# Optimization experiments

Measured on AMD Instinct MI355X. Metric: run time of the kernel, lower is better.

## Reference

```python
import jax, jax.numpy as jnp
import numpy as np

N = 8192
D = 128
AVG_DEG = 32


def setup_inputs() -> dict:
    key = jax.random.key(0)
    ks = jax.random.split(key, 10)
    Z = jax.random.normal(ks[0], (N, D), dtype=jnp.float32)
    # random symmetric binary adjacency with avg degree ~ AVG_DEG
    p = AVG_DEG / N
    adj = (jax.random.uniform(ks[1], (N, N)) < p).astype(jnp.float32)
    adj = jnp.maximum(adj, adj.T)
    # symmetric normalized adjacency: D^{-1/2} A D^{-1/2}
    deg = adj.sum(axis=1)
    d_inv_sqrt = jnp.where(deg > 0, 1.0 / jnp.sqrt(deg), 0.0)
    A_norm = d_inv_sqrt[:, None] * adj * d_inv_sqrt[None, :]
    sc = 1.0 / np.sqrt(D)
    W_D = jax.random.uniform(ks[2], (D, D), minval=-sc, maxval=sc, dtype=jnp.float32)
    W_C = jax.random.uniform(ks[3], (D, D), minval=-sc, maxval=sc, dtype=jnp.float32)
    w_V = jax.random.uniform(ks[4], (D,), minval=-sc, maxval=sc, dtype=jnp.float32)
    W1 = jax.random.uniform(ks[5], (D, D), minval=-sc, maxval=sc, dtype=jnp.float32)
    b1 = jax.random.uniform(ks[6], (D,), minval=-sc, maxval=sc, dtype=jnp.float32)
    W2 = jax.random.uniform(ks[7], (D, D), minval=-sc, maxval=sc, dtype=jnp.float32)
    b2 = jax.random.uniform(ks[8], (D,), minval=-sc, maxval=sc, dtype=jnp.float32)
    omega_logit = jnp.float32(0.0)  # sigmoid -> 0.5
    delta_logit = jnp.float32(0.0)
    return {"Z": Z, "A_norm": A_norm, "W_D": W_D, "W_C": W_C, "w_V": w_V,
            "W1": W1, "b1": b1, "W2": W2, "b2": b2,
            "omega_logit": omega_logit, "delta_logit": delta_logit}


def reference(Z, A_norm, W_D, W_C, w_V, W1, b1, W2, b2, omega_logit, delta_logit):
    omega = jax.nn.sigmoid(omega_logit)
    delta = jax.nn.sigmoid(delta_logit)
    # Diffusion: ReLU(A_norm @ Z @ W_D^T)
    dif = jax.nn.relu(A_norm @ (Z @ W_D.T))  # [N, D]
    # Convection (standard attention). Since W_V is D->1,
    # W_V(z_i - z_j) == s_i - s_j with s = Z @ w_V -> avoid [N,N,D] tensor.
    s = Z @ w_V                                   # [N]
    V_bar = jax.nn.sigmoid(s[:, None] - s[None, :])  # [N, N]
    A = jax.nn.softmax(V_bar, axis=1)                # row-stochastic [N, N]
    con = A @ (Z @ W_C.T)                            # [N, D]
    # Reaction: nonlinear MLP
    rea = jnp.tanh(Z @ W1.T + b1) @ W2.T + b2        # [N, D]
    return omega * dif + (1.0 - omega) * con + delta * rea
```

## Files before the change

### kernel.cpp

```cpp
#include <hip/hip_runtime.h>
#include <hip/hip_bf16.h>
#include <stdint.h>

#define NN 8192
#define DD 128
#define MAXDEG 128

typedef float f32x4 __attribute__((ext_vector_type(4)));
typedef __bf16 bf16x8 __attribute__((ext_vector_type(8)));
typedef __bf16 bf16x4 __attribute__((ext_vector_type(4)));

__device__ __forceinline__ f32x4 mfma16(bf16x8 a, bf16x8 b, f32x4 c) {
    return __builtin_amdgcn_mfma_f32_16x16x32_bf16(a, b, c, 0, 0, 0);
}

__device__ __forceinline__ bf16x8 pack8(f32x4 lo, f32x4 hi) {
    bf16x8 r;
    r[0] = (__bf16)lo[0]; r[1] = (__bf16)lo[1]; r[2] = (__bf16)lo[2]; r[3] = (__bf16)lo[3];
    r[4] = (__bf16)hi[0]; r[5] = (__bf16)hi[1]; r[6] = (__bf16)hi[2]; r[7] = (__bf16)hi[3];
    return r;
}

__device__ __forceinline__ float fast_sigmoid(float x) {
    return __builtin_amdgcn_rcpf(1.0f + __expf(-x));
}

__device__ __forceinline__ uint32_t f32_bf16bits_rne(float f) {
    union { float f; uint32_t u; } c; c.f = f;
    return (c.u + 0x7fffu + ((c.u >> 16) & 1u)) >> 16;
}

__device__ __forceinline__ float bf16bits_f32(uint32_t b) {
    union { uint32_t u; float f; } c; c.u = b << 16;
    return c.f;
}

__global__ __launch_bounds__(256) void k_prep_sE(
    const float* __restrict__ Z, const float* __restrict__ wV, float* __restrict__ E)
{
    const int wid  = threadIdx.x >> 6;
    const int lane = threadIdx.x & 63;
    const int row  = blockIdx.x * 4 + wid;
    float p = Z[row * DD + lane] * wV[lane] + Z[row * DD + 64 + lane] * wV[64 + lane];
    #pragma unroll
    for (int off = 32; off > 0; off >>= 1) p += __shfl_xor(p, off, 64);
    if (lane == 0) E[row] = __expf(p);
}

__global__ __launch_bounds__(256) void k_conv_w(
    const float* __restrict__ W_D, const float* __restrict__ W_C,
    const float* __restrict__ W1, const float* __restrict__ W2,
    __bf16* __restrict__ Wb)
{
    const int t = blockIdx.x * 256 + threadIdx.x;
    const int m = t >> 12, i = t & 4095;
    const float* src = (m == 0) ? W_D : (m == 1) ? W_C : (m == 2) ? W1 : W2;
    const f32x4 v = *(const f32x4*)(src + i * 4);
    bf16x4 b;
    b[0] = (__bf16)v[0]; b[1] = (__bf16)v[1]; b[2] = (__bf16)v[2]; b[3] = (__bf16)v[3];
    *(bf16x4*)(Wb + m * 16384 + i * 4) = b;
}

__global__ __launch_bounds__(256) void k_prep2(
    const float* __restrict__ Z, const __bf16* __restrict__ Wb,
    const float* __restrict__ b1, const float* __restrict__ b2,
    const float* __restrict__ delta_logit,
    __bf16* __restrict__ XR, __bf16* __restrict__ YB, __bf16* __restrict__ REA)
{
    __shared__ __bf16 Hs[32][136];
    const int tid = threadIdx.x;
    const int w = tid >> 6, l = tid & 63;
    const int lr = l & 15, lg = l >> 4;
    const int wr = w & 1, wn = w >> 1;
    const int r0 = blockIdx.x * 32;
    const int arow = r0 + 16 * wr + lr;
    const __bf16* WDb = Wb;
    const __bf16* WCb = Wb + 16384;
    const __bf16* W1b = Wb + 32768;
    const __bf16* W2b = Wb + 49152;

    const f32x4 zero4 = {0.f, 0.f, 0.f, 0.f};
    f32x4 aXD[4], aY[4], aH[4];
    #pragma unroll
    for (int i = 0; i < 4; ++i) { aXD[i] = zero4; aY[i] = zero4; aH[i] = zero4; }

    #pragma unroll
    for (int t = 0; t < 4; ++t) {
        const int k0 = 32 * t + 8 * lg;
        const bf16x8 af = pack8(*(const f32x4*)(Z + arow * DD + k0),
                                *(const f32x4*)(Z + arow * DD + k0 + 4));
        #pragma unroll
        for (int nf = 0; nf < 4; ++nf) {
            const int col = 64 * wn + 16 * nf + lr;
            aXD[nf] = mfma16(af, *(const bf16x8*)(WDb + col * DD + k0), aXD[nf]);
            aY[nf]  = mfma16(af, *(const bf16x8*)(WCb + col * DD + k0), aY[nf]);
            aH[nf]  = mfma16(af, *(const bf16x8*)(W1b + col * DD + k0), aH[nf]);
        }
    }

    const int orow = r0 + 16 * wr + 4 * lg;
    const int tile = orow >> 5;
    #pragma unroll
    for (int nf = 0; nf < 4; ++nf) {
        const int col = 64 * wn + 16 * nf + lr;
        bf16x4 yo;
        const float bb1 = b1[col];
        #pragma unroll
        for (int r = 0; r < 4; ++r) {
            XR[(orow + r) * DD + col] = (__bf16)aXD[nf][r];
            yo[r] = (__bf16)aY[nf][r];
            const float x = aH[nf][r] + bb1;
            const float e = __expf(2.0f * x);
            Hs[16 * wr + 4 * lg + r][col] = (__bf16)(1.0f - 2.0f * __builtin_amdgcn_rcpf(e + 1.0f));
        }
        *(bf16x4*)(YB + tile * 4096 + col * 32 + (orow & 31)) = yo;
    }
    __syncthreads();

    f32x4 aR[4];
    #pragma unroll
    for (int i = 0; i < 4; ++i) aR[i] = zero4;
    #pragma unroll
    for (int t = 0; t < 4; ++t) {
        const int k0 = 32 * t + 8 * lg;
        const bf16x8 hf = *(const bf16x8*)(&Hs[16 * wr + lr][k0]);
        #pragma unroll
        for (int nf = 0; nf < 4; ++nf) {
            const int col = 64 * wn + 16 * nf + lr;
            aR[nf] = mfma16(hf, *(const bf16x8*)(W2b + col * DD + k0), aR[nf]);
        }
    }
    const float delta = fast_sigmoid(delta_logit[0]);
    #pragma unroll
    for (int nf = 0; nf < 4; ++nf) {
        const int col = 64 * wn + 16 * nf + lr;
        const float bb2 = b2[col];
        #pragma unroll
        for (int r = 0; r < 4; ++r)
            REA[(orow + r) * DD + col] = (__bf16)(delta * (aR[nf][r] + bb2));
    }
}

__global__ __launch_bounds__(256) void k_scan(
    const float* __restrict__ A, uint32_t* __restrict__ cnt, uint32_t* __restrict__ ents)
{
    const int g = blockIdx.x * 256 + threadIdx.x;
    #pragma unroll 4
    for (int i = 0; i < 32; ++i) {
        const int idx4 = i * 524288 + g;
        const f32x4 v = *(const f32x4*)(A + (size_t)idx4 * 4);
        const float sm = (v[0] + v[1]) + (v[2] + v[3]);
        if (sm != 0.0f) {
            const int row = idx4 >> 11;
            const int colbase = (idx4 & 2047) * 4;
            #pragma unroll
            for (int k = 0; k < 4; ++k) {
                if (v[k] != 0.0f) {
                    const uint32_t slot = atomicAdd(&cnt[row], 1u);
                    if (slot < MAXDEG)
                        ents[row * MAXDEG + slot] =
                            ((uint32_t)(colbase + k) << 16) | f32_bf16bits_rne(v[k]);
                }
            }
        }
    }
}

__global__ __launch_bounds__(512) __attribute__((amdgpu_waves_per_eu(2, 2))) void k_con(
    const float* __restrict__ E, const __bf16* __restrict__ YB,
    const __bf16* __restrict__ XR, const __bf16* __restrict__ REA,
    const uint32_t* __restrict__ cnt, const uint32_t* __restrict__ ents,
    const float* __restrict__ omega_logit, float* __restrict__ out)
{
    __shared__ float red[4][64][76];
    float* conS = &red[0][0][0];
    const int tid = threadIdx.x;
    const int w = tid >> 6, l = tid & 63;
    const int lr = l & 15, lg = l >> 4;
    const int r0 = blockIdx.x * 32;
    const int kstart = w * 1024;

    const float* ep = E + kstart + 8 * lg;
    const __bf16* yp = YB + (kstart >> 5) * 4096 + lr * 32 + 8 * lg;
    const float u0 = E[r0 + lr];
    const float u1 = E[r0 + 16 + lr];

    const f32x4 zero4 = {0.f, 0.f, 0.f, 0.f};
    f32x4 aC0[8], aC1[8], aden0 = zero4, aden1 = zero4;
    #pragma unroll
    for (int i = 0; i < 8; ++i) { aC0[i] = zero4; aC1[i] = zero4; }
    bf16x8 ones;
    #pragma unroll
    for (int i = 0; i < 8; ++i) ones[i] = (__bf16)1.0f;

    f32x4 eAa, eBa, eAb, eBb;
    bf16x8 bya[8], byb[8];
    intptr_t adv = 32;

#define LOADT(S) do {                                                         \
        eA##S = *(const f32x4*)(ep); eB##S = *(const f32x4*)(ep + 4);         \
        _Pragma("unroll")                                                     \
        for (int c = 0; c < 8; ++c) by##S[c] = *(const bf16x8*)(yp + c * 512);\
        ep += adv; yp += adv * 128;                                           \
    } while (0)

#define COMPT(S) do {                                                         \
        bf16x8 gf0, gf1;                                                      \
        _Pragma("unroll")                                                     \
        for (int j = 0; j < 4; ++j) {                                         \
            const float ea = eA##S[j], eb = eB##S[j];                         \
            gf0[j]     = (__bf16)__expf(u0 * __builtin_amdgcn_rcpf(u0 + ea)); \
            gf0[4 + j] = (__bf16)__expf(u0 * __builtin_amdgcn_rcpf(u0 + eb)); \
            gf1[j]     = (__bf16)__expf(u1 * __builtin_amdgcn_rcpf(u1 + ea)); \
            gf1[4 + j] = (__bf16)__expf(u1 * __builtin_amdgcn_rcpf(u1 + eb)); \
        }                                                                     \
        _Pragma("unroll")                                                     \
        for (int c = 0; c < 8; ++c) {                                         \
            aC0[c] = mfma16(gf0, by##S[c], aC0[c]);                           \
            aC1[c] = mfma16(gf1, by##S[c], aC1[c]);                           \
        }                                                                     \
        aden0 = mfma16(gf0, ones, aden0);                                     \
        aden1 = mfma16(gf1, ones, aden1);                                     \
    } while (0)

    LOADT(a);
    for (int it = 0; it < 16; ++it) {
        if (it == 15) adv = 0;
        LOADT(b); COMPT(a);
        LOADT(a); COMPT(b);
    }
#undef LOADT
#undef COMPT

#define STORE_ACC(dst) do {                                                   \
        _Pragma("unroll")                                                     \
        for (int c = 0; c < 8; ++c) {                                         \
            *(f32x4*)((dst) + c * 4)      = aC0[c];                           \
            *(f32x4*)((dst) + 36 + c * 4) = aC1[c];                           \
        }                                                                     \
        *(f32x4*)((dst) + 32)      = aden0;                                   \
        *(f32x4*)((dst) + 36 + 32) = aden1;                                   \
    } while (0)
#define ADD_ACC(src) do {                                                     \
        _Pragma("unroll")                                                     \
        for (int c = 0; c < 8; ++c) {                                         \
            aC0[c] += *(const f32x4*)((src) + c * 4);                         \
            aC1[c] += *(const f32x4*)((src) + 36 + c * 4);                    \
        }                                                                     \
        aden0 += *(const f32x4*)((src) + 32);                                 \
        aden1 += *(const f32x4*)((src) + 36 + 32);                            \
    } while (0)

    if (w >= 4) STORE_ACC(&red[w - 4][l][0]);
    __syncthreads();
    if (w < 4) ADD_ACC(&red[w][l][0]);
    __syncthreads();
    if (w == 2 || w == 3) STORE_ACC(&red[w - 2][l][0]);
    __syncthreads();
    if (w < 2) ADD_ACC(&red[w][l][0]);
    __syncthreads();
    if (w == 1) STORE_ACC(&red[0][l][0]);
    __syncthreads();
    if (w == 0) {
        ADD_ACC(&red[0][l][0]);
        __builtin_amdgcn_s_barrier();
        #pragma unroll
        for (int rf = 0; rf < 2; ++rf) {
            #pragma unroll
            for (int c = 0; c < 8; ++c) {
                const f32x4 v = rf ? aC1[c] : aC0[c];
                #pragma unroll
                for (int r = 0; r < 4; ++r)
                    conS[(16 * rf + 4 * lg + r) * 132 + 16 * c + lr] = v[r];
            }
            if (lr == 0) {
                const f32x4 d = rf ? aden1 : aden0;
                #pragma unroll
                for (int r = 0; r < 4; ++r)
                    conS[32 * 132 + 16 * rf + 4 * lg + r] = d[r];
            }
        }
    } else {
        __builtin_amdgcn_s_barrier();
    }
    __syncthreads();

    const int row = tid >> 4;
    const int g16 = tid & 15;
    const int col0 = 8 * g16;
    const int rg = r0 + row;
    float acc[8];
    #pragma unroll
    for (int i = 0; i < 8; ++i) acc[i] = 0.0f;

    const uint32_t n = min(cnt[rg], (uint32_t)MAXDEG);
    const uint32_t* ep2 = ents + rg * MAXDEG;
    for (uint32_t e = 0; e < n; ++e) {
        const uint32_t p = ep2[e];
        const float val = bf16bits_f32(p & 0xffffu);
        const bf16x8 xv = *(const bf16x8*)(XR + (size_t)(p >> 16) * DD + col0);
        #pragma unroll
        for (int i = 0; i < 8; ++i) acc[i] += val * (float)xv[i];
    }

    const float omega = fast_sigmoid(omega_logit[0]);
    const float om1 = 1.0f - omega;
    const float dinv = __builtin_amdgcn_rcpf(conS[32 * 132 + row]);
    const bf16x8 rea8 = *(const bf16x8*)(REA + (size_t)rg * DD + col0);
    f32x4 o0, o1;
    #pragma unroll
    for (int i = 0; i < 8; ++i) {
        const float dv = fmaxf(acc[i], 0.0f);
        const float cv = conS[row * 132 + col0 + i] * dinv;
        const float v = (float)rea8[i] + omega * dv + om1 * cv;
        if (i < 4) o0[i] = v; else o1[i - 4] = v;
    }
    *(f32x4*)(out + (size_t)rg * DD + col0) = o0;
    *(f32x4*)(out + (size_t)rg * DD + col0 + 4) = o1;
}

extern "C" void kernel_launch(void* const* d_in, const int* in_sizes, int n_in,
                              void* d_out, int out_size, void* d_ws, size_t ws_size,
                              hipStream_t stream) {
    (void)in_sizes; (void)n_in; (void)out_size; (void)ws_size;
    const float* Z   = (const float*)d_in[0];
    const float* A   = (const float*)d_in[1];
    const float* W_D = (const float*)d_in[2];
    const float* W_C = (const float*)d_in[3];
    const float* wV  = (const float*)d_in[4];
    const float* W1  = (const float*)d_in[5];
    const float* b1  = (const float*)d_in[6];
    const float* W2  = (const float*)d_in[7];
    const float* b2  = (const float*)d_in[8];
    const float* omega_logit = (const float*)d_in[9];
    const float* delta_logit = (const float*)d_in[10];
    float* out = (float*)d_out;

    char* wsb = (char*)d_ws;
    float*    E    = (float*)wsb;
    __bf16*   Wb   = (__bf16*)(wsb + 32768);
    __bf16*   XR   = (__bf16*)(wsb + 163840);
    __bf16*   YB   = (__bf16*)(wsb + 163840 + 2097152);
    __bf16*   REA  = (__bf16*)(wsb + 163840 + 2 * 2097152);
    uint32_t* cnt  = (uint32_t*)(wsb + 163840 + 3 * 2097152);
    uint32_t* ents = (uint32_t*)(wsb + 163840 + 3 * 2097152 + 32768);

    (void)hipMemsetAsync(cnt, 0, 8192 * sizeof(uint32_t), stream);
    k_prep_sE<<<dim3(2048), dim3(256), 0, stream>>>(Z, wV, E);
    k_conv_w<<<dim3(64), dim3(256), 0, stream>>>(W_D, W_C, W1, W2, Wb);
    k_prep2<<<dim3(256), dim3(256), 0, stream>>>(Z, Wb, b1, b2, delta_logit, XR, YB, REA);
    k_scan<<<dim3(2048), dim3(256), 0, stream>>>(A, cnt, ents);
    k_con<<<dim3(256), dim3(512), 0, stream>>>(E, YB, XR, REA, cnt, ents, omega_logit, out);
}
```

Before: 512.8 us.

## Scan adjacency one row per wave with ballot compaction; unroll sparse gather

The adjacency scan now assigns one wavefront per row and compacts nonzeros with ballot and mbcnt prefix counts, so it no longer needs a global atomicAdd for each nonzero. The row count is written once at the end, which makes the memset of the count array unnecessary. The sparse diffusion gather loop is unrolled by four with a vectorized entry load to expose more memory-level parallelism. Entries within a row now come out in sorted column order, and each wave issues ballots even for all-zero chunks, which adds some instructions to a scan that is dominated by dense reads.

```diff
diff --git a/kernel.cpp b/kernel.cpp
--- a/kernel.cpp
+++ b/kernel.cpp
@@ -7,6 +7,7 @@
 #define MAXDEG 128
 
 typedef float f32x4 __attribute__((ext_vector_type(4)));
+typedef unsigned int u32x4 __attribute__((ext_vector_type(4)));
 typedef __bf16 bf16x8 __attribute__((ext_vector_type(8)));
 typedef __bf16 bf16x4 __attribute__((ext_vector_type(4)));
 
@@ -144,26 +145,30 @@
 __global__ __launch_bounds__(256) void k_scan(
     const float* __restrict__ A, uint32_t* __restrict__ cnt, uint32_t* __restrict__ ents)
 {
-    const int g = blockIdx.x * 256 + threadIdx.x;
+    const int wid = threadIdx.x >> 6, lane = threadIdx.x & 63;
+    const int row = blockIdx.x * 4 + wid;
+    const float* rp = A + (size_t)row * NN + lane * 4;
+    uint32_t* eb = ents + row * MAXDEG;
+    uint32_t base = 0;
     #pragma unroll 4
     for (int i = 0; i < 32; ++i) {
-        const int idx4 = i * 524288 + g;
-        const f32x4 v = *(const f32x4*)(A + (size_t)idx4 * 4);
-        const float sm = (v[0] + v[1]) + (v[2] + v[3]);
-        if (sm != 0.0f) {
-            const int row = idx4 >> 11;
-            const int colbase = (idx4 & 2047) * 4;
-            #pragma unroll
-            for (int k = 0; k < 4; ++k) {
-                if (v[k] != 0.0f) {
-                    const uint32_t slot = atomicAdd(&cnt[row], 1u);
-                    if (slot < MAXDEG)
-                        ents[row * MAXDEG + slot] =
-                            ((uint32_t)(colbase + k) << 16) | f32_bf16bits_rne(v[k]);
-                }
+        const f32x4 v = *(const f32x4*)(rp + i * 256);
+        const int colb = i * 256 + lane * 4;
+        #pragma unroll
+        for (int k = 0; k < 4; ++k) {
+            const bool nz = (v[k] != 0.0f);
+            const unsigned long long m = __ballot(nz);
+            if (nz) {
+                const uint32_t pfx = __builtin_amdgcn_mbcnt_hi(
+                    (uint32_t)(m >> 32), __builtin_amdgcn_mbcnt_lo((uint32_t)m, 0u));
+                const uint32_t slot = base + pfx;
+                if (slot < MAXDEG)
+                    eb[slot] = ((uint32_t)(colb + k) << 16) | f32_bf16bits_rne(v[k]);
             }
-        }
-    }
+            base += (uint32_t)__popcll(m);
+        }
+    }
+    if (lane == 0) cnt[row] = base;
 }
 
 __global__ __launch_bounds__(512) __attribute__((amdgpu_waves_per_eu(2, 2))) void k_con(
@@ -295,7 +300,23 @@
 
     const uint32_t n = min(cnt[rg], (uint32_t)MAXDEG);
     const uint32_t* ep2 = ents + rg * MAXDEG;
-    for (uint32_t e = 0; e < n; ++e) {
+    uint32_t e = 0;
+    for (; e + 4 <= n; e += 4) {
+        const u32x4 p = *(const u32x4*)(ep2 + e);
+        const bf16x8 x0 = *(const bf16x8*)(XR + (size_t)(p[0] >> 16) * DD + col0);
+        const bf16x8 x1 = *(const bf16x8*)(XR + (size_t)(p[1] >> 16) * DD + col0);
+        const bf16x8 x2 = *(const bf16x8*)(XR + (size_t)(p[2] >> 16) * DD + col0);
+        const bf16x8 x3 = *(const bf16x8*)(XR + (size_t)(p[3] >> 16) * DD + col0);
+        const float v0 = bf16bits_f32(p[0] & 0xffffu);
+        const float v1 = bf16bits_f32(p[1] & 0xffffu);
+        const float v2 = bf16bits_f32(p[2] & 0xffffu);
+        const float v3 = bf16bits_f32(p[3] & 0xffffu);
+        #pragma unroll
+        for (int i = 0; i < 8; ++i)
+            acc[i] += v0 * (float)x0[i] + v1 * (float)x1[i]
+                    + v2 * (float)x2[i] + v3 * (float)x3[i];
+    }
+    for (; e < n; ++e) {
         const uint32_t p = ep2[e];
         const float val = bf16bits_f32(p & 0xffffu);
         const bf16x8 xv = *(const bf16x8*)(XR + (size_t)(p >> 16) * DD + col0);
@@ -345,7 +366,6 @@
     uint32_t* cnt  = (uint32_t*)(wsb + 163840 + 3 * 2097152);
     uint32_t* ents = (uint32_t*)(wsb + 163840 + 3 * 2097152 + 32768);
 
-    (void)hipMemsetAsync(cnt, 0, 8192 * sizeof(uint32_t), stream);
     k_prep_sE<<<dim3(2048), dim3(256), 0, stream>>>(Z, wV, E);
     k_conv_w<<<dim3(64), dim3(256), 0, stream>>>(W_D, W_C, W1, W2, Wb);
     k_prep2<<<dim3(256), dim3(256), 0, stream>>>(Z, Wb, b1, b2, delta_logit, XR, YB, REA);
```

Measured after the change: 453.7 us. -11.5%, faster.
